# Kernel tuning notes

Hardware: AMD Instinct MI355X
Metric: run time of the kernel (lower is better)

The kernel has to match this reference:

```python
import jax, jax.numpy as jnp
import numpy as np

B_, S, D_IN, D_OUT, R = 4, 2048, 4096, 4096, 16


def setup_inputs() -> dict:
    key = jax.random.key(0)
    kx, ka, kb = jax.random.split(key, 3)
    x = jax.random.normal(kx, (B_, S, D_IN), dtype=jnp.float32)
    A = jax.random.normal(ka, (D_IN, R), dtype=jnp.float32) * 0.02
    B = jax.random.normal(kb, (R, D_OUT), dtype=jnp.float32) * 0.02
    return {"x": x, "A": A, "B": B}


def reference(x, A, B):
    # Faithful to the original: materialize the low-rank product A@B
    # ([in_features, out_features]) first, then apply it to x.
    # (Note: the original forward ignores self.scaling.)
    W = A @ B  # [D_IN, D_OUT]
    return x @ W  # [B, S, D_OUT]
```

## Files before the change

kernel.cpp:

```cpp
#include <hip/hip_runtime.h>
#include <stdint.h>


#define KD 4096
#define ND 4096
#define NR 16
#define BLK 256
#define MB 8
#define NCHUNK 512

#define FMA4(ACC, XV, A4)                         \
    ACC.x = fmaf((XV), (A4).x, ACC.x);            \
    ACC.y = fmaf((XV), (A4).y, ACC.y);            \
    ACC.z = fmaf((XV), (A4).z, ACC.z);            \
    ACC.w = fmaf((XV), (A4).w, ACC.w);

#define RED1(C, OFF) C += __shfl_xor(C, OFF, 64);
#define RED(OFF)                                  \
    RED1(acc0.x, OFF) RED1(acc0.y, OFF)           \
    RED1(acc0.z, OFF) RED1(acc0.w, OFF)           \
    RED1(acc1.x, OFF) RED1(acc1.y, OFF)           \
    RED1(acc1.z, OFF) RED1(acc1.w, OFF)

#define FMAB(TV, R)                                                        \
    {                                                                      \
        const float4 b_ = *reinterpret_cast<const float4*>(bp + (R) * NCHUNK); \
        o.x = fmaf((TV), b_.x, o.x);                                       \
        o.y = fmaf((TV), b_.y, o.y);                                       \
        o.z = fmaf((TV), b_.z, o.z);                                       \
        o.w = fmaf((TV), b_.w, o.w);                                       \
    }

__global__ __launch_bounds__(BLK)
void lora_fused(const float* __restrict__ X,
                const float* __restrict__ A,
                const float* __restrict__ Bm,
                float* __restrict__ O)
{
    __shared__ float t_s[MB][NR];
    __shared__ float bs[NR * NCHUNK];

    const int tid  = threadIdx.x;
    const int wv   = tid >> 6;
    const int lane = tid & 63;
    const int rq   = lane & 3;
    const int kg   = lane >> 2;
    const size_t m0 = (size_t)blockIdx.x * MB;

    const float* xp0 = X + (m0 + 2 * wv) * (size_t)KD + kg;
    const float* xp1 = xp0 + KD;
    const float* ap  = A + (size_t)kg * NR + rq * 4;

    float4 acc0 = {0.f, 0.f, 0.f, 0.f};
    float4 acc1 = {0.f, 0.f, 0.f, 0.f};

    #pragma unroll 4
    for (int t = 0; t < KD / 16; ++t) {
        const float  x0 = xp0[(size_t)t * 16];
        const float  x1 = xp1[(size_t)t * 16];
        const float4 a  = *reinterpret_cast<const float4*>(ap + (size_t)t * (16 * NR));
        FMA4(acc0, x0, a)
        FMA4(acc1, x1, a)
    }

    RED(4) RED(8) RED(16) RED(32)

    if (lane < 4) {
        *reinterpret_cast<float4*>(&t_s[2 * wv + 0][lane * 4]) = acc0;
        *reinterpret_cast<float4*>(&t_s[2 * wv + 1][lane * 4]) = acc1;
    }
    __syncthreads();

    const int m  = tid >> 5;
    const int cs = tid & 31;

    const float4 t0 = *reinterpret_cast<const float4*>(&t_s[m][0]);
    const float4 t1 = *reinterpret_cast<const float4*>(&t_s[m][4]);
    const float4 t2 = *reinterpret_cast<const float4*>(&t_s[m][8]);
    const float4 t3 = *reinterpret_cast<const float4*>(&t_s[m][12]);

    float* op = O + (m0 + m) * (size_t)ND;

    #pragma unroll 1
    for (int cc = 0; cc < ND / NCHUNK; ++cc) {
        #pragma unroll
        for (int i = 0; i < 8; ++i) {
            const int p   = i * BLK + tid;
            const int row = p >> 7;
            const int c4  = p & 127;
            const float4 v = *reinterpret_cast<const float4*>(
                Bm + (size_t)row * ND + cc * NCHUNK + c4 * 4);
            *reinterpret_cast<float4*>(&bs[p * 4]) = v;
        }
        __syncthreads();

        #pragma unroll
        for (int j = 0; j < 4; ++j) {
            const int c4 = cs + 32 * j;
            const float* bp = &bs[c4 * 4];
            float4 o = {0.f, 0.f, 0.f, 0.f};
            FMAB(t0.x, 0)  FMAB(t0.y, 1)  FMAB(t0.z, 2)  FMAB(t0.w, 3)
            FMAB(t1.x, 4)  FMAB(t1.y, 5)  FMAB(t1.z, 6)  FMAB(t1.w, 7)
            FMAB(t2.x, 8)  FMAB(t2.y, 9)  FMAB(t2.z, 10) FMAB(t2.w, 11)
            FMAB(t3.x, 12) FMAB(t3.y, 13) FMAB(t3.z, 14) FMAB(t3.w, 15)
            *reinterpret_cast<float4*>(op + cc * NCHUNK + c4 * 4) = o;
        }
        __syncthreads();
    }
}

extern "C" void kernel_launch(void* const* d_in, const int* in_sizes, int n_in,
                              void* d_out, int out_size, void* d_ws, size_t ws_size,
                              hipStream_t stream) {
    const float* X  = (const float*)d_in[0];
    const float* A  = (const float*)d_in[1];
    const float* Bm = (const float*)d_in[2];
    float* O = (float*)d_out;
    lora_fused<<<8192 / MB, BLK, 0, stream>>>(X, A, Bm, O);
}
```

Baseline: 303.1 us.

## Vectorize X loads with prefetch and share B reads across two rows

The x·A reduction now has each lane load a float4 of four consecutive k values, with a register prefetch of the next X vector, in place of strided scalar loads. Each lane uses four A float4 vectors per step. In the second stage each wave computes two output rows at once, so every B float4 read from shared memory feeds two rows of FMAs, halving LDS traffic per output. The unroll of the B staging loop is reduced to 2. The aim is fewer, wider global loads and less LDS bandwidth, at the cost of more registers per thread.

```diff
diff --git a/kernel.cpp b/kernel.cpp
--- a/kernel.cpp
+++ b/kernel.cpp
@@ -9,26 +9,26 @@
 #define MB 8
 #define NCHUNK 512
 
-#define FMA4(ACC, XV, A4)                         \
-    ACC.x = fmaf((XV), (A4).x, ACC.x);            \
-    ACC.y = fmaf((XV), (A4).y, ACC.y);            \
-    ACC.z = fmaf((XV), (A4).z, ACC.z);            \
-    ACC.w = fmaf((XV), (A4).w, ACC.w);
+#define FMA4(ACC, XS, A4)                          \
+    ACC.x = fmaf((XS), (A4).x, ACC.x);             \
+    ACC.y = fmaf((XS), (A4).y, ACC.y);             \
+    ACC.z = fmaf((XS), (A4).z, ACC.z);             \
+    ACC.w = fmaf((XS), (A4).w, ACC.w);
 
 #define RED1(C, OFF) C += __shfl_xor(C, OFF, 64);
-#define RED(OFF)                                  \
-    RED1(acc0.x, OFF) RED1(acc0.y, OFF)           \
-    RED1(acc0.z, OFF) RED1(acc0.w, OFF)           \
-    RED1(acc1.x, OFF) RED1(acc1.y, OFF)           \
+#define RED(OFF)                                   \
+    RED1(acc0.x, OFF) RED1(acc0.y, OFF)            \
+    RED1(acc0.z, OFF) RED1(acc0.w, OFF)            \
+    RED1(acc1.x, OFF) RED1(acc1.y, OFF)            \
     RED1(acc1.z, OFF) RED1(acc1.w, OFF)
 
-#define FMAB(TV, R)                                                        \
-    {                                                                      \
+#define FMAB2(TA, TB, R)                                                       \
+    {                                                                          \
         const float4 b_ = *reinterpret_cast<const float4*>(bp + (R) * NCHUNK); \
-        o.x = fmaf((TV), b_.x, o.x);                                       \
-        o.y = fmaf((TV), b_.y, o.y);                                       \
-        o.z = fmaf((TV), b_.z, o.z);                                       \
-        o.w = fmaf((TV), b_.w, o.w);                                       \
+        oa.x = fmaf((TA), b_.x, oa.x);  ob.x = fmaf((TB), b_.x, ob.x);         \
+        oa.y = fmaf((TA), b_.y, oa.y);  ob.y = fmaf((TB), b_.y, ob.y);         \
+        oa.z = fmaf((TA), b_.z, oa.z);  ob.z = fmaf((TB), b_.z, ob.z);         \
+        oa.w = fmaf((TA), b_.w, oa.w);  ob.w = fmaf((TB), b_.w, ob.w);         \
     }
 
 __global__ __launch_bounds__(BLK)
@@ -44,23 +44,39 @@
     const int wv   = tid >> 6;
     const int lane = tid & 63;
     const int rq   = lane & 3;
-    const int kg   = lane >> 2;
+    const int kq   = lane >> 2;
     const size_t m0 = (size_t)blockIdx.x * MB;
 
-    const float* xp0 = X + (m0 + 2 * wv) * (size_t)KD + kg;
+    const float* xp0 = X + (m0 + 2 * wv) * (size_t)KD + kq * 4;
     const float* xp1 = xp0 + KD;
-    const float* ap  = A + (size_t)kg * NR + rq * 4;
+    const float* ap  = A + (size_t)kq * 4 * NR + rq * 4;
 
     float4 acc0 = {0.f, 0.f, 0.f, 0.f};
     float4 acc1 = {0.f, 0.f, 0.f, 0.f};
 
-    #pragma unroll 4
-    for (int t = 0; t < KD / 16; ++t) {
-        const float  x0 = xp0[(size_t)t * 16];
-        const float  x1 = xp1[(size_t)t * 16];
-        const float4 a  = *reinterpret_cast<const float4*>(ap + (size_t)t * (16 * NR));
-        FMA4(acc0, x0, a)
-        FMA4(acc1, x1, a)
+    float4 nx0 = *reinterpret_cast<const float4*>(xp0);
+    float4 nx1 = *reinterpret_cast<const float4*>(xp1);
+
+    #pragma unroll 1
+    for (int t = 0; t < KD / 64; ++t) {
+        const float4 x0 = nx0;
+        const float4 x1 = nx1;
+
+        const float* at = ap + (size_t)t * (64 * NR);
+        const float4 a0 = *reinterpret_cast<const float4*>(at);
+        const float4 a1 = *reinterpret_cast<const float4*>(at + NR);
+        const float4 a2 = *reinterpret_cast<const float4*>(at + 2 * NR);
+        const float4 a3 = *reinterpret_cast<const float4*>(at + 3 * NR);
+
+        if (t < KD / 64 - 1) {
+            nx0 = *reinterpret_cast<const float4*>(xp0 + (size_t)(t + 1) * 64);
+            nx1 = *reinterpret_cast<const float4*>(xp1 + (size_t)(t + 1) * 64);
+        }
+
+        FMA4(acc0, x0.x, a0)  FMA4(acc1, x1.x, a0)
+        FMA4(acc0, x0.y, a1)  FMA4(acc1, x1.y, a1)
+        FMA4(acc0, x0.z, a2)  FMA4(acc1, x1.z, a2)
+        FMA4(acc0, x0.w, a3)  FMA4(acc1, x1.w, a3)
     }
 
     RED(4) RED(8) RED(16) RED(32)
@@ -71,39 +87,48 @@
     }
     __syncthreads();
 
-    const int m  = tid >> 5;
-    const int cs = tid & 31;
-
-    const float4 t0 = *reinterpret_cast<const float4*>(&t_s[m][0]);
-    const float4 t1 = *reinterpret_cast<const float4*>(&t_s[m][4]);
-    const float4 t2 = *reinterpret_cast<const float4*>(&t_s[m][8]);
-    const float4 t3 = *reinterpret_cast<const float4*>(&t_s[m][12]);
-
-    float* op = O + (m0 + m) * (size_t)ND;
+    const int m = 2 * wv;
+    float* opa = O + (m0 + m) * (size_t)ND;
+    float* opb = opa + ND;
 
     #pragma unroll 1
     for (int cc = 0; cc < ND / NCHUNK; ++cc) {
-        #pragma unroll
+        #pragma unroll 2
         for (int i = 0; i < 8; ++i) {
             const int p   = i * BLK + tid;
             const int row = p >> 7;
             const int c4  = p & 127;
-            const float4 v = *reinterpret_cast<const float4*>(
-                Bm + (size_t)row * ND + cc * NCHUNK + c4 * 4);
-            *reinterpret_cast<float4*>(&bs[p * 4]) = v;
+            *reinterpret_cast<float4*>(&bs[p * 4]) =
+                *reinterpret_cast<const float4*>(
+                    Bm + (size_t)row * ND + cc * NCHUNK + c4 * 4);
         }
         __syncthreads();
 
+        const float4 ta0 = *reinterpret_cast<const float4*>(&t_s[m][0]);
+        const float4 ta1 = *reinterpret_cast<const float4*>(&t_s[m][4]);
+        const float4 ta2 = *reinterpret_cast<const float4*>(&t_s[m][8]);
+        const float4 ta3 = *reinterpret_cast<const float4*>(&t_s[m][12]);
+        const float4 tb0 = *reinterpret_cast<const float4*>(&t_s[m + 1][0]);
+        const float4 tb1 = *reinterpret_cast<const float4*>(&t_s[m + 1][4]);
+        const float4 tb2 = *reinterpret_cast<const float4*>(&t_s[m + 1][8]);
+        const float4 tb3 = *reinterpret_cast<const float4*>(&t_s[m + 1][12]);
+
         #pragma unroll
-        for (int j = 0; j < 4; ++j) {
-            const int c4 = cs + 32 * j;
+        for (int j = 0; j < 2; ++j) {
+            const int c4 = lane + 64 * j;
             const float* bp = &bs[c4 * 4];
-            float4 o = {0.f, 0.f, 0.f, 0.f};
-            FMAB(t0.x, 0)  FMAB(t0.y, 1)  FMAB(t0.z, 2)  FMAB(t0.w, 3)
-            FMAB(t1.x, 4)  FMAB(t1.y, 5)  FMAB(t1.z, 6)  FMAB(t1.w, 7)
-            FMAB(t2.x, 8)  FMAB(t2.y, 9)  FMAB(t2.z, 10) FMAB(t2.w, 11)
-            FMAB(t3.x, 12) FMAB(t3.y, 13) FMAB(t3.z, 14) FMAB(t3.w, 15)
-            *reinterpret_cast<float4*>(op + cc * NCHUNK + c4 * 4) = o;
+            float4 oa = {0.f, 0.f, 0.f, 0.f};
+            float4 ob = {0.f, 0.f, 0.f, 0.f};
+            FMAB2(ta0.x, tb0.x, 0)  FMAB2(ta0.y, tb0.y, 1)
+            FMAB2(ta0.z, tb0.z, 2)  FMAB2(ta0.w, tb0.w, 3)
+            FMAB2(ta1.x, tb1.x, 4)  FMAB2(ta1.y, tb1.y, 5)
+            FMAB2(ta1.z, tb1.z, 6)  FMAB2(ta1.w, tb1.w, 7)
+            FMAB2(ta2.x, tb2.x, 8)  FMAB2(ta2.y, tb2.y, 9)
+            FMAB2(ta2.z, tb2.z, 10) FMAB2(ta2.w, tb2.w, 11)
+            FMAB2(ta3.x, tb3.x, 12) FMAB2(ta3.y, tb3.y, 13)
+            FMAB2(ta3.z, tb3.z, 14) FMAB2(ta3.w, tb3.w, 15)
+            *reinterpret_cast<float4*>(opa + cc * NCHUNK + c4 * 4) = oa;
+            *reinterpret_cast<float4*>(opb + cc * NCHUNK + c4 * 4) = ob;
         }
         __syncthreads();
     }
```

Result: slower. 329.8 us (+8.8%).
